# Kernel tuning notes

Hardware: AMD Instinct MI355X
Metric: run time of the kernel (lower is better)

The kernel has to match this reference:

```python
import jax, jax.numpy as jnp
import numpy as np

Z_DIM = 2  # state dimension is hard-coded (fc1: Linear(2, H), fc3: Linear(H, 2))


def _mlp(z, W1, b1, W2, b2, W3, b3):
    # torch.nn.Linear: y = x @ W.T + b
    h = jax.nn.elu(z @ W1.T + b1)
    h = jax.nn.elu(h @ W2.T + b2)
    return h @ W3.T + b3


def setup_inputs() -> dict:
    key = jax.random.key(0)
    ks = jax.random.split(key, 8)
    B, H = 1_000_000, 64
    s_in = 1.0 / np.sqrt(Z_DIM)
    s_h = 1.0 / np.sqrt(H)
    u = lambda k, shp, s: jax.random.uniform(k, shp, jnp.float32, -s, s)
    return {
        "t": jax.random.normal(ks[0], (1,), jnp.float32),
        "z_and_logp": jax.random.normal(ks[1], (B, Z_DIM + 1), jnp.float32),
        "W1": u(ks[2], (H, Z_DIM), s_in),
        "b1": u(ks[3], (H,), s_in),
        "W2": u(ks[4], (H, H), s_h),
        "b2": u(ks[5], (H,), s_h),
        "W3": u(ks[6], (Z_DIM, H), s_h),
        "b3": u(ks[7], (Z_DIM,), s_h),
    }


def reference(t, z_and_logp, W1, b1, W2, b2, W3, b3):
    # t is an unused time argument (ODE solver interface).
    z = z_and_logp[:, :Z_DIM]  # [B, 2]; logp column is not used in forward
    f = lambda x: _mlp(x, W1, b1, W2, b2, W3, b3)

    # Exact Jacobian trace via forward-mode JVPs with unit tangents (Z_DIM=2,
    # so this small fixed loop mirrors the per-dim autograd loop in torch).
    dz_dt = None
    trace = jnp.zeros(z.shape[0], dtype=z.dtype)
    for i in range(Z_DIM):
        e = jnp.zeros_like(z).at[:, i].set(1.0)
        out, jz = jax.jvp(f, (z,), (e,))
        if dz_dt is None:
            dz_dt = out
        trace = trace + jz[:, i]

    dlogp_dt = -trace[:, None]  # [B, 1]
    return jnp.concatenate([dz_dt, dlogp_dt], axis=1)  # [B, 3]
```

## Files before the change

kernel.cpp:

```cpp
#include <hip/hip_runtime.h>
#include <hip/hip_bf16.h>


typedef short bf16x8 __attribute__((ext_vector_type(8)));
typedef float f32x4  __attribute__((ext_vector_type(4)));

static __device__ __forceinline__ short f2bf(float x) {
    __hip_bfloat16 b = __float2bfloat16(x);
    return __builtin_bit_cast(short, b);
}

__global__ __launch_bounds__(256) __attribute__((amdgpu_waves_per_eu(3, 3)))
void odefunc_mfma(const float* __restrict__ zin,
                  const float* __restrict__ W1, const float* __restrict__ b1,
                  const float* __restrict__ W2, const float* __restrict__ b2,
                  const float* __restrict__ W3, const float* __restrict__ b3,
                  float* __restrict__ out, int B, int ntiles)
{
    __shared__ f32x4 sC[96];

    const int lane = threadIdx.x & 63;
    const int quad = lane >> 4;
    const int col  = lane & 15;

    if (threadIdx.x < 64) {
        int i = threadIdx.x;
        float* s = (float*)sC;
        s[i]       = W1[2*i];
        s[64 + i]  = W1[2*i + 1];
        s[128 + i] = b1[i];
        s[192 + i] = b2[i];
        s[256 + i] = W3[i];
        s[320 + i] = W3[64 + i];
    }

    const int wid    = blockIdx.x * (blockDim.x >> 6) + (threadIdx.x >> 6);
    const int nwaves = gridDim.x * (blockDim.x >> 6);

    bf16x8 aW2[4][2];
#pragma unroll
    for (int mt = 0; mt < 4; ++mt)
#pragma unroll
        for (int jt = 0; jt < 2; ++jt) {
            const float* p = W2 + (mt * 16 + col) * 64 + jt * 32 + quad * 8;
#pragma unroll
            for (int jj = 0; jj < 8; ++jj) aW2[mt][jt][jj] = f2bf(p[jj]);
        }

    const float b30 = b3[0], b31 = b3[1];
    const f32x4 zero4 = {0.f, 0.f, 0.f, 0.f};

    __syncthreads();

    const int lload = lane < 48 ? lane : 47;
    int t = wid;
    float zv = 0.f;
    if (t < ntiles) zv = zin[t * 48 + lload];

    int cofs = 0;
    for (; t < ntiles; t += nwaves) {
        asm volatile("" : "+v"(cofs));

        int tn = t + nwaves;
        int tc = tn < ntiles ? tn : t;
        float zvn = zin[tc * 48 + lload];

        float z0 = __shfl(zv, 3 * col);
        float z1 = __shfl(zv, 3 * col + 1);

        bf16x8 Ah[2], Au[2], Av[2];
#pragma unroll
        for (int jt = 0; jt < 2; ++jt) {
            int j4 = cofs + jt * 8 + quad * 2;
            f32x4 w0a = sC[j4],      w0b = sC[j4 + 1];
            f32x4 w1a = sC[j4 + 16], w1b = sC[j4 + 17];
            f32x4 bba = sC[j4 + 32], bbb = sC[j4 + 33];
#pragma unroll
            for (int jj = 0; jj < 8; ++jj) {
                float w0 = (jj < 4) ? w0a[jj & 3] : w0b[jj & 3];
                float w1 = (jj < 4) ? w1a[jj & 3] : w1b[jj & 3];
                float bb = (jj < 4) ? bba[jj & 3] : bbb[jj & 3];
                float a  = fmaf(w0, z0, fmaf(w1, z1, bb));
                float ex = __expf(fminf(a, 0.f));
                float h  = fmaxf(a, 0.f) + (ex - 1.f);
                Ah[jt][jj] = f2bf(h);
                Au[jt][jj] = f2bf(ex * w0);
                Av[jt][jj] = f2bf(ex * w1);
            }
        }

        f32x4 accH[4], accU[4], accV[4];
#pragma unroll
        for (int mt = 0; mt < 4; ++mt) {
            accH[mt] = __builtin_amdgcn_mfma_f32_16x16x32_bf16(aW2[mt][0], Ah[0], zero4, 0, 0, 0);
            accH[mt] = __builtin_amdgcn_mfma_f32_16x16x32_bf16(aW2[mt][1], Ah[1], accH[mt], 0, 0, 0);
            accU[mt] = __builtin_amdgcn_mfma_f32_16x16x32_bf16(aW2[mt][0], Au[0], zero4, 0, 0, 0);
            accU[mt] = __builtin_amdgcn_mfma_f32_16x16x32_bf16(aW2[mt][1], Au[1], accU[mt], 0, 0, 0);
            accV[mt] = __builtin_amdgcn_mfma_f32_16x16x32_bf16(aW2[mt][0], Av[0], zero4, 0, 0, 0);
            accV[mt] = __builtin_amdgcn_mfma_f32_16x16x32_bf16(aW2[mt][1], Av[1], accV[mt], 0, 0, 0);
        }

        float o0 = 0.f, o1 = 0.f, trc = 0.f;
#pragma unroll
        for (int mt = 0; mt < 4; ++mt) {
            int k4 = cofs + 48 + mt * 4 + quad;
            f32x4 b2v = sC[k4];
            f32x4 w30 = sC[k4 + 16];
            f32x4 w31 = sC[k4 + 32];
#pragma unroll
            for (int i = 0; i < 4; ++i) {
                float a2  = accH[mt][i] + b2v[i];
                float ex2 = __expf(fminf(a2, 0.f));
                float hh  = fmaxf(a2, 0.f) + (ex2 - 1.f);
                o0  = fmaf(w30[i], hh, o0);
                o1  = fmaf(w31[i], hh, o1);
                trc = fmaf(ex2, fmaf(w30[i], accU[mt][i], w31[i] * accV[mt][i]), trc);
            }
        }

        o0  += __shfl_xor(o0, 16);  o0  += __shfl_xor(o0, 32);
        o1  += __shfl_xor(o1, 16);  o1  += __shfl_xor(o1, 32);
        trc += __shfl_xor(trc, 16); trc += __shfl_xor(trc, 32);

        int row = t * 16 + col;
        if (lane < 16 && row < B) {
            out[3 * row + 0] = o0 + b30;
            out[3 * row + 1] = o1 + b31;
            out[3 * row + 2] = -trc;
        }

        zv = zvn;
    }
}

extern "C" void kernel_launch(void* const* d_in, const int* in_sizes, int n_in,
                              void* d_out, int out_size, void* d_ws, size_t ws_size,
                              hipStream_t stream) {
    const float* zin = (const float*)d_in[1];
    const float* W1  = (const float*)d_in[2];
    const float* b1  = (const float*)d_in[3];
    const float* W2  = (const float*)d_in[4];
    const float* b2  = (const float*)d_in[5];
    const float* W3  = (const float*)d_in[6];
    const float* b3  = (const float*)d_in[7];
    float* out = (float*)d_out;

    int B = in_sizes[1] / 3;
    int ntiles = (B + 15) / 16;
    int grid = 1536;
    odefunc_mfma<<<grid, 256, 0, stream>>>(zin, W1, b1, W2, b2, W3, b3,
                                           out, B, ntiles);
}
```

Before: 137.6 us.

## Fold W3 and W1 into a precomputed trace weight matrix, halving tangent MFMAs

Rewrites the Jacobian-trace computation algebraically. A per-wave matrix G[k][j] = W2[k][j]*(W3[0][k]*W1[j][0] + W3[1][k]*W1[j][1]) is precomputed, so the trace needs only one MFMA chain over the layer-1 ELU derivative instead of two tangent chains (U and V). It also packs bf16 conversions with v_cvt_pk_bf16_f32. This cuts MFMA work per tile from 24 to 16 and removes two bf16 operand builds per element, at the cost of extra registers for the G fragments and a different bf16 rounding point for the trace.

Result: faster. 128.9 us (-6.3%).

```diff
diff --git a/kernel.cpp b/kernel.cpp
--- a/kernel.cpp
+++ b/kernel.cpp
@@ -4,10 +4,17 @@
 
 typedef short bf16x8 __attribute__((ext_vector_type(8)));
 typedef float f32x4  __attribute__((ext_vector_type(4)));
+typedef int   i32x4  __attribute__((ext_vector_type(4)));
 
 static __device__ __forceinline__ short f2bf(float x) {
     __hip_bfloat16 b = __float2bfloat16(x);
     return __builtin_bit_cast(short, b);
+}
+
+static __device__ __forceinline__ int cvt_pk_bf16(float lo, float hi) {
+    int r;
+    asm("v_cvt_pk_bf16_f32 %0, %1, %2" : "=v"(r) : "v"(lo), "v"(hi));
+    return r;
 }
 
 __global__ __launch_bounds__(256) __attribute__((amdgpu_waves_per_eu(3, 3)))
@@ -37,15 +44,23 @@
     const int wid    = blockIdx.x * (blockDim.x >> 6) + (threadIdx.x >> 6);
     const int nwaves = gridDim.x * (blockDim.x >> 6);
 
-    bf16x8 aW2[4][2];
+    bf16x8 aW2[4][2], aG[4][2];
 #pragma unroll
-    for (int mt = 0; mt < 4; ++mt)
+    for (int mt = 0; mt < 4; ++mt) {
+        const int k = mt * 16 + col;
+        const float ck = W3[k], dk = W3[64 + k];
 #pragma unroll
         for (int jt = 0; jt < 2; ++jt) {
-            const float* p = W2 + (mt * 16 + col) * 64 + jt * 32 + quad * 8;
+            const float* p = W2 + k * 64 + jt * 32 + quad * 8;
 #pragma unroll
-            for (int jj = 0; jj < 8; ++jj) aW2[mt][jt][jj] = f2bf(p[jj]);
+            for (int jj = 0; jj < 8; ++jj) {
+                int j = jt * 32 + quad * 8 + jj;
+                float w2 = p[jj];
+                aW2[mt][jt][jj] = f2bf(w2);
+                aG[mt][jt][jj]  = f2bf(w2 * fmaf(ck, W1[2*j], dk * W1[2*j+1]));
+            }
         }
+    }
 
     const float b30 = b3[0], b31 = b3[1];
     const f32x4 zero4 = {0.f, 0.f, 0.f, 0.f};
@@ -68,36 +83,41 @@
         float z0 = __shfl(zv, 3 * col);
         float z1 = __shfl(zv, 3 * col + 1);
 
-        bf16x8 Ah[2], Au[2], Av[2];
+        bf16x8 Bh[2], Bex[2];
 #pragma unroll
         for (int jt = 0; jt < 2; ++jt) {
             int j4 = cofs + jt * 8 + quad * 2;
             f32x4 w0a = sC[j4],      w0b = sC[j4 + 1];
             f32x4 w1a = sC[j4 + 16], w1b = sC[j4 + 17];
             f32x4 bba = sC[j4 + 32], bbb = sC[j4 + 33];
+            float h[8], ex[8];
 #pragma unroll
             for (int jj = 0; jj < 8; ++jj) {
                 float w0 = (jj < 4) ? w0a[jj & 3] : w0b[jj & 3];
                 float w1 = (jj < 4) ? w1a[jj & 3] : w1b[jj & 3];
                 float bb = (jj < 4) ? bba[jj & 3] : bbb[jj & 3];
                 float a  = fmaf(w0, z0, fmaf(w1, z1, bb));
-                float ex = __expf(fminf(a, 0.f));
-                float h  = fmaxf(a, 0.f) + (ex - 1.f);
-                Ah[jt][jj] = f2bf(h);
-                Au[jt][jj] = f2bf(ex * w0);
-                Av[jt][jj] = f2bf(ex * w1);
+                float e  = __expf(fminf(a, 0.f));
+                ex[jj] = e;
+                h[jj]  = fmaxf(a, 0.f) + (e - 1.f);
             }
+            i32x4 ph, pe;
+#pragma unroll
+            for (int d = 0; d < 4; ++d) {
+                ph[d] = cvt_pk_bf16(h[2*d],  h[2*d+1]);
+                pe[d] = cvt_pk_bf16(ex[2*d], ex[2*d+1]);
+            }
+            Bh[jt]  = __builtin_bit_cast(bf16x8, ph);
+            Bex[jt] = __builtin_bit_cast(bf16x8, pe);
         }
 
-        f32x4 accH[4], accU[4], accV[4];
+        f32x4 accH[4], accT[4];
 #pragma unroll
         for (int mt = 0; mt < 4; ++mt) {
-            accH[mt] = __builtin_amdgcn_mfma_f32_16x16x32_bf16(aW2[mt][0], Ah[0], zero4, 0, 0, 0);
-            accH[mt] = __builtin_amdgcn_mfma_f32_16x16x32_bf16(aW2[mt][1], Ah[1], accH[mt], 0, 0, 0);
-            accU[mt] = __builtin_amdgcn_mfma_f32_16x16x32_bf16(aW2[mt][0], Au[0], zero4, 0, 0, 0);
-            accU[mt] = __builtin_amdgcn_mfma_f32_16x16x32_bf16(aW2[mt][1], Au[1], accU[mt], 0, 0, 0);
-            accV[mt] = __builtin_amdgcn_mfma_f32_16x16x32_bf16(aW2[mt][0], Av[0], zero4, 0, 0, 0);
-            accV[mt] = __builtin_amdgcn_mfma_f32_16x16x32_bf16(aW2[mt][1], Av[1], accV[mt], 0, 0, 0);
+            accH[mt] = __builtin_amdgcn_mfma_f32_16x16x32_bf16(aW2[mt][0], Bh[0], zero4, 0, 0, 0);
+            accH[mt] = __builtin_amdgcn_mfma_f32_16x16x32_bf16(aW2[mt][1], Bh[1], accH[mt], 0, 0, 0);
+            accT[mt] = __builtin_amdgcn_mfma_f32_16x16x32_bf16(aG[mt][0], Bex[0], zero4, 0, 0, 0);
+            accT[mt] = __builtin_amdgcn_mfma_f32_16x16x32_bf16(aG[mt][1], Bex[1], accT[mt], 0, 0, 0);
         }
 
         float o0 = 0.f, o1 = 0.f, trc = 0.f;
@@ -110,11 +130,11 @@
 #pragma unroll
             for (int i = 0; i < 4; ++i) {
                 float a2  = accH[mt][i] + b2v[i];
-                float ex2 = __expf(fminf(a2, 0.f));
-                float hh  = fmaxf(a2, 0.f) + (ex2 - 1.f);
+                float e2  = __expf(fminf(a2, 0.f));
+                float hh  = fmaxf(a2, 0.f) + (e2 - 1.f);
                 o0  = fmaf(w30[i], hh, o0);
                 o1  = fmaf(w31[i], hh, o1);
-                trc = fmaf(ex2, fmaf(w30[i], accU[mt][i], w31[i] * accV[mt][i]), trc);
+                trc = fmaf(e2, accT[mt][i], trc);
             }
         }
 
```
